# Kernel optimization log

Hardware: AMD Instinct MI355X
Metric: run time of the kernel (lower is better)

The kernel has to match this reference:

```python
import jax, jax.numpy as jnp
import numpy as np

B, S, D = 2, 2048, 1024
H, DQK, DV = 16, 64, 64
DECAY = 0.85


def _fractal_weights(seq_len: int, decay: float) -> np.ndarray:
    # Dragon-curve hierarchical weights: earlier (coarser) positions get higher
    # weight; weight decays by `decay` per hierarchy level. Normalized to sum 1,
    # matching DragonCurveGenerator.get_hierarchical_weights semantics.
    idx = np.arange(seq_len)
    level = np.floor(np.log2(idx + 1)).astype(np.int32)
    w = decay ** level.astype(np.float32)
    return (w / w.sum()).astype(np.float32)


def setup_inputs() -> dict:
    key = jax.random.key(0)
    kx, kq, kk, kv, ko = jax.random.split(key, 5)
    s = 1.0 / np.sqrt(D)
    return {
        "x": jax.random.normal(kx, (B, S, D), dtype=jnp.float32),
        "Wq": jax.random.normal(kq, (D, H * DQK), dtype=jnp.float32) * s,
        "Wk": jax.random.normal(kk, (D, H * DQK), dtype=jnp.float32) * s,
        "Wv": jax.random.normal(kv, (D, H * DV), dtype=jnp.float32) * s,
        "Wo": jax.random.normal(ko, (H * DV, D), dtype=jnp.float32) * s,
        "fractal_weights": jnp.asarray(_fractal_weights(S, DECAY)),
    }


def reference(x, Wq, Wk, Wv, Wo, fractal_weights):
    b, s, _ = x.shape
    # Projections (Linear with bias=False); weights stored as (in, out).
    Q = (x @ Wq).reshape(b, s, H, DQK).transpose(0, 2, 1, 3)  # [B,H,S,Dqk]
    K = (x @ Wk).reshape(b, s, H, DQK).transpose(0, 2, 1, 3)
    V = (x @ Wv).reshape(b, s, H, DV).transpose(0, 2, 1, 3)   # [B,H,S,Dv]
    scale = 1.0 / jnp.sqrt(jnp.asarray(DQK, dtype=x.dtype))
    scores = jnp.einsum("bhqd,bhkd->bhqk", Q, K) * scale      # [B,H,S,S]
    # Multiplicative per-key fractal bias applied BEFORE softmax.
    scores = scores * fractal_weights[None, None, None, :]
    attn = jax.nn.softmax(scores, axis=-1)
    out = jnp.einsum("bhqk,bhkd->bhqd", attn, V)               # [B,H,S,Dv]
    out = out.transpose(0, 2, 1, 3).reshape(b, s, H * DV)
    return out @ Wo                                            # [B,S,D]
```

## Files before the change

kernel.cpp:

```cpp
#include <hip/hip_runtime.h>
#include <hip/hip_bf16.h>
#include <stdint.h>

#define B_  2
#define S_  2048
#define D_  1024
#define H_  16
#define DH_ 64

typedef __attribute__((ext_vector_type(8))) __bf16    bf16x8;
typedef __attribute__((ext_vector_type(8))) _Float16  f16x8;
typedef __attribute__((ext_vector_type(2))) __fp16    fp16x2;
typedef __attribute__((ext_vector_type(4))) float     f32x4;

__device__ inline unsigned short f2bf(float f) {
    union { float f; uint32_t u; } v; v.f = f;
    uint32_t r = (v.u + 0x7fffu + ((v.u >> 16) & 1u)) >> 16;
    return (unsigned short)r;
}

__device__ __forceinline__ void g2l16(const unsigned short* g, unsigned short* l) {
    __builtin_amdgcn_global_load_lds(
        (const __attribute__((address_space(1))) unsigned int*)g,
        (__attribute__((address_space(3))) unsigned int*)l,
        16, 0, 0);
}


__global__ void convert_x(const float* __restrict__ x, unsigned short* __restrict__ xb, int n) {
    int i = (blockIdx.x * blockDim.x + threadIdx.x) * 4;
    if (i < n) {
        float4 v = *(const float4*)(x + i);
        ushort4 o;
        o.x = f2bf(v.x); o.y = f2bf(v.y); o.z = f2bf(v.z); o.w = f2bf(v.w);
        *(ushort4*)(xb + i) = o;
    }
}

__global__ void transpose_w(const float* __restrict__ s0, const float* __restrict__ s1,
                            const float* __restrict__ s2, const float* __restrict__ s3,
                            unsigned short* __restrict__ d0, unsigned short* __restrict__ d1,
                            unsigned short* __restrict__ d2, unsigned short* __restrict__ d3) {
    __shared__ float tile[32][33];
    const float* src; unsigned short* dst;
    switch (blockIdx.z) {
        case 0: src = s0; dst = d0; break;
        case 1: src = s1; dst = d1; break;
        case 2: src = s2; dst = d2; break;
        default: src = s3; dst = d3; break;
    }
    int n0 = blockIdx.x * 32, k0 = blockIdx.y * 32;
    int tx = threadIdx.x, ty = threadIdx.y;
    for (int j = 0; j < 32; j += 8)
        tile[ty + j][tx] = src[(long)(k0 + ty + j) * 1024 + n0 + tx];
    __syncthreads();
    for (int j = 0; j < 32; j += 8)
        dst[(long)(n0 + ty + j) * 1024 + k0 + tx] = f2bf(tile[tx][ty + j]);
}

template<int MODE>
__global__ __launch_bounds__(256, 2)
void gemm128(const unsigned short* __restrict__ A, const unsigned short* __restrict__ Bt,
             unsigned short* __restrict__ Qo, unsigned short* __restrict__ Ko,
             unsigned short* __restrict__ Vt, float* __restrict__ Cout)
{
    __shared__ __align__(16) unsigned short As[128 * 64];
    __shared__ __align__(16) unsigned short Bs[128 * 64];
    const int tid  = threadIdx.x;
    const int lane = tid & 63, wid = tid >> 6;
    const int quad = lane >> 4, l15 = lane & 15;
    const int wm = wid >> 1, wn = wid & 1;
    const int bm = blockIdx.y, bn = blockIdx.x;
    const int K = 1024;
    f32x4 acc[4][4] = {};
    const long Abase = (long)bm * 128 * K;
    const long Bbase = (long)bn * 128 * K;

    for (int k0 = 0; k0 < K; k0 += 64) {
        __syncthreads();
#pragma unroll
        for (int i = 0; i < 4; i++) {
            int slot = i * 256 + wid * 64 + lane;
            int row = slot >> 3, cp = slot & 7;
            int c = cp ^ (row & 7);
            g2l16(A + Abase + (long)row * K + k0 + c * 8, &As[(i * 256 + wid * 64) * 8]);
        }
#pragma unroll
        for (int i = 0; i < 4; i++) {
            int slot = i * 256 + wid * 64 + lane;
            int row = slot >> 3, cp = slot & 7;
            int c = cp ^ (row & 7);
            g2l16(Bt + Bbase + (long)row * K + k0 + c * 8, &Bs[(i * 256 + wid * 64) * 8]);
        }
        __syncthreads();
#pragma unroll
        for (int ks = 0; ks < 2; ks++) {
            bf16x8 af[4], bfr[4];
#pragma unroll
            for (int t = 0; t < 4; t++) {
                int ra = wm * 64 + t * 16 + l15;
                af[t]  = *(const bf16x8*)(As + ra * 64 + (((ks * 4 + quad) ^ (l15 & 7))) * 8);
                int rb = wn * 64 + t * 16 + l15;
                bfr[t] = *(const bf16x8*)(Bs + rb * 64 + (((ks * 4 + quad) ^ (l15 & 7))) * 8);
            }
#pragma unroll
            for (int tm = 0; tm < 4; tm++)
#pragma unroll
                for (int tn = 0; tn < 4; tn++)
                    acc[tm][tn] = __builtin_amdgcn_mfma_f32_16x16x32_bf16(af[tm], bfr[tn], acc[tm][tn], 0, 0, 0);
        }
    }

    const float Cq = 0.125f * 1.44269504f;
    for (int tm = 0; tm < 4; tm++)
        for (int tn = 0; tn < 4; tn++)
            for (int r = 0; r < 4; r++) {
                int gm = bm * 128 + wm * 64 + tm * 16 + quad * 4 + r;
                int gn = bn * 128 + wn * 64 + tn * 16 + l15;
                float v = acc[tm][tn][r];
                if (MODE == 0) {
                    int b = gm >> 11, s = gm & 2047;
                    if (gn < 1024) {
                        int h = gn >> 6, d = gn & 63;
                        Qo[(((long)(b * H_ + h) * S_ + s) << 6) + d] = f2bf(v * Cq);
                    } else if (gn < 2048) {
                        int g = gn - 1024; int h = g >> 6, d = g & 63;
                        Ko[(((long)(b * H_ + h) * S_ + s) << 6) + d] = f2bf(v);
                    } else {
                        int g = gn - 2048; int h = g >> 6, d = g & 63;
                        union { _Float16 h; unsigned short u; } cv;
                        cv.h = (_Float16)v;
                        Vt[((long)(b * H_ + h) * DH_ + d) * S_ + s] = cv.u;
                    }
                } else {
                    Cout[(long)gm * 1024 + gn] = v;
                }
            }
}

__global__ __launch_bounds__(256, 3)
void attn_kernel(const unsigned short* __restrict__ Q, const unsigned short* __restrict__ Kb,
                 const unsigned short* __restrict__ Vt, const float* __restrict__ fw,
                 unsigned short* __restrict__ O)
{
    __shared__ __align__(16) unsigned short Ks[2][64 * 64];
    __shared__ __align__(16) unsigned short Vs[2][64 * 64];
    __shared__ __align__(16) unsigned short P[4][32 * 72];

    const int tid  = threadIdx.x;
    const int lane = tid & 63, wid = tid >> 6;
    const int quad = lane >> 4, l15 = lane & 15;
    const int bh = blockIdx.y;
    const int qt = blockIdx.x;

    const unsigned short* Kg = Kb + (long)bh * S_ * DH_;
    const unsigned short* Vg = Vt + (long)bh * (long)DH_ * S_;

    bf16x8 qf[2][2];
#pragma unroll
    for (int s = 0; s < 2; s++) {
        const unsigned short* Qp = Q + ((long)bh * S_ + qt * 128 + wid * 32 + s * 16 + l15) * DH_ + quad * 8;
        qf[s][0] = *(const bf16x8*)(Qp);
        qf[s][1] = *(const bf16x8*)(Qp + 32);
    }

    auto issue = [&](int buf, int kt) {
#pragma unroll
        for (int i = 0; i < 2; i++) {
            int slot = wid * 128 + i * 64 + lane;
            int row = slot >> 3, cp = slot & 7;
            int c = cp ^ (row & 7);
            g2l16(Kg + ((long)(kt * 64 + row) * 64 + c * 8), &Ks[buf][(wid * 128 + i * 64) * 8]);
        }
#pragma unroll
        for (int i = 0; i < 2; i++) {
            int slot = wid * 128 + i * 64 + lane;
            int row = slot >> 3, cp = slot & 7;
            int c = cp ^ (row & 7);
            g2l16(Vg + ((long)row * S_ + kt * 64 + c * 8), &Vs[buf][(wid * 128 + i * 64) * 8]);
        }
    };

    f32x4 oacc[2][4] = {};
    float l_r[2] = {0.f, 0.f};

    issue(0, 0);
    __syncthreads();

    for (int kt = 0; kt < S_ / 64; kt++) {
        const int cur = kt & 1;
        if (kt + 1 < S_ / 64) issue(1 - cur, kt + 1);

        f32x4 wvc[4];
#pragma unroll
        for (int t = 0; t < 4; t++) {
            float4 w = *(const float4*)(fw + kt * 64 + t * 16 + quad * 4);
            wvc[t][0] = w.x; wvc[t][1] = w.y; wvc[t][2] = w.z; wvc[t][3] = w.w;
        }

        const unsigned short* Kc = &Ks[cur][0];
        const unsigned short* Vc = &Vs[cur][0];

        f32x4 sacc[2][4] = {};
#pragma unroll
        for (int t = 0; t < 4; t++) {
            int row = t * 16 + l15;
            bf16x8 k0 = *(const bf16x8*)(Kc + (row * 8 + (quad       ^ (l15 & 7))) * 8);
            bf16x8 k1 = *(const bf16x8*)(Kc + (row * 8 + ((4 + quad) ^ (l15 & 7))) * 8);
#pragma unroll
            for (int s = 0; s < 2; s++) {
                sacc[s][t] = __builtin_amdgcn_mfma_f32_16x16x32_bf16(k0, qf[s][0], sacc[s][t], 0, 0, 0);
                sacc[s][t] = __builtin_amdgcn_mfma_f32_16x16x32_bf16(k1, qf[s][1], sacc[s][t], 0, 0, 0);
            }
        }

        unsigned short* pb = &P[wid][0];
#pragma unroll
        for (int s = 0; s < 2; s++) {
#pragma unroll
            for (int t = 0; t < 4; t++) {
                float p0 = __builtin_amdgcn_exp2f(sacc[s][t][0] * wvc[t][0]);
                float p1 = __builtin_amdgcn_exp2f(sacc[s][t][1] * wvc[t][1]);
                float p2 = __builtin_amdgcn_exp2f(sacc[s][t][2] * wvc[t][2]);
                float p3 = __builtin_amdgcn_exp2f(sacc[s][t][3] * wvc[t][3]);
                l_r[s] += (p0 + p1) + (p2 + p3);
                union { fp16x2 h; unsigned int u; } a, b;
                a.h = __builtin_amdgcn_cvt_pkrtz(p0, p1);
                b.h = __builtin_amdgcn_cvt_pkrtz(p2, p3);
                *(uint2*)(pb + (s * 16 + l15) * 72 + t * 16 + quad * 4) = make_uint2(a.u, b.u);
            }
        }

#pragma unroll
        for (int ks = 0; ks < 2; ks++) {
            f16x8 pf0 = *(const f16x8*)(pb + l15 * 72 + ks * 32 + quad * 8);
            f16x8 pf1 = *(const f16x8*)(pb + (16 + l15) * 72 + ks * 32 + quad * 8);
#pragma unroll
            for (int t = 0; t < 4; t++) {
                int row = t * 16 + l15;
                f16x8 vf = *(const f16x8*)(Vc + (row * 8 + ((ks * 4 + quad) ^ (l15 & 7))) * 8);
                oacc[0][t] = __builtin_amdgcn_mfma_f32_16x16x32_f16(pf0, vf, oacc[0][t], 0, 0, 0);
                oacc[1][t] = __builtin_amdgcn_mfma_f32_16x16x32_f16(pf1, vf, oacc[1][t], 0, 0, 0);
            }
        }

        __syncthreads();
    }

#pragma unroll
    for (int s = 0; s < 2; s++) {
        l_r[s] += __shfl_xor(l_r[s], 16);
        l_r[s] += __shfl_xor(l_r[s], 32);
    }

    int b = bh >> 4, h = bh & 15;
#pragma unroll
    for (int s = 0; s < 2; s++)
#pragma unroll
        for (int r = 0; r < 4; r++) {
            float inv = 1.0f / __shfl(l_r[s], quad * 4 + r);
            int srow = qt * 128 + wid * 32 + s * 16 + quad * 4 + r;
#pragma unroll
            for (int t = 0; t < 4; t++)
                O[((long)(b * S_ + srow)) * 1024 + h * DH_ + t * 16 + l15] = f2bf(oacc[s][t][r] * inv);
        }
}


extern "C" void kernel_launch(void* const* d_in, const int* in_sizes, int n_in,
                              void* d_out, int out_size, void* d_ws, size_t ws_size,
                              hipStream_t stream)
{
    const float* x  = (const float*)d_in[0];
    const float* Wq = (const float*)d_in[1];
    const float* Wk = (const float*)d_in[2];
    const float* Wv = (const float*)d_in[3];
    const float* Wo = (const float*)d_in[4];
    const float* fw = (const float*)d_in[5];
    float* out = (float*)d_out;

    char* ws = (char*)d_ws;
    unsigned short* xb    = (unsigned short*)(ws);
    unsigned short* WqkvT = (unsigned short*)(ws + 8388608);
    unsigned short* WoT   = (unsigned short*)(ws + 14680064);
    unsigned short* Qb    = (unsigned short*)(ws + 16777216);
    unsigned short* Kb    = (unsigned short*)(ws + 25165824);
    unsigned short* Vt    = (unsigned short*)(ws + 33554432);
    unsigned short* Ob    = xb;

    convert_x<<<dim3((B_ * S_ * D_) / 4 / 256), dim3(256), 0, stream>>>(x, xb, B_ * S_ * D_);
    transpose_w<<<dim3(32, 32, 4), dim3(32, 8), 0, stream>>>(
        Wq, Wk, Wv, Wo,
        WqkvT, WqkvT + 1024 * 1024, WqkvT + 2 * 1024 * 1024, WoT);
    gemm128<0><<<dim3(24, 32), dim3(256), 0, stream>>>(xb, WqkvT, Qb, Kb, Vt, (float*)nullptr);
    attn_kernel<<<dim3(S_ / 128, B_ * H_), dim3(256), 0, stream>>>(Qb, Kb, Vt, fw, Ob);
    gemm128<1><<<dim3(8, 32), dim3(256), 0, stream>>>(Ob, WoT,
        (unsigned short*)nullptr, (unsigned short*)nullptr, (unsigned short*)nullptr, out);
}
```

Before: 208.2 us.

## Use two waves per attention block, each handling 64 query rows

The attention block drops from four waves to two, and each wave now processes 64 query rows instead of 32. K fragments are loaded from LDS once per tile and reused across four query subtiles, and each V fragment feeds four MFMAs, which cuts LDS reads per FLOP. The cost is fewer waves per block and more accumulator registers per thread (oacc 4x4), and the launch bounds change to (128,1). Occupancy and latency hiding may drop, and each wave now carries more of the global-to-LDS copy work.

```diff
diff --git a/kernel.cpp b/kernel.cpp
--- a/kernel.cpp
+++ b/kernel.cpp
@@ -138,14 +138,14 @@
             }
 }
 
-__global__ __launch_bounds__(256, 3)
+__global__ __launch_bounds__(128, 1)
 void attn_kernel(const unsigned short* __restrict__ Q, const unsigned short* __restrict__ Kb,
                  const unsigned short* __restrict__ Vt, const float* __restrict__ fw,
                  unsigned short* __restrict__ O)
 {
     __shared__ __align__(16) unsigned short Ks[2][64 * 64];
     __shared__ __align__(16) unsigned short Vs[2][64 * 64];
-    __shared__ __align__(16) unsigned short P[4][32 * 72];
+    __shared__ __align__(16) unsigned short P[2][64 * 72];
 
     const int tid  = threadIdx.x;
     const int lane = tid & 63, wid = tid >> 6;
@@ -156,33 +156,35 @@
     const unsigned short* Kg = Kb + (long)bh * S_ * DH_;
     const unsigned short* Vg = Vt + (long)bh * (long)DH_ * S_;
 
-    bf16x8 qf[2][2];
-#pragma unroll
-    for (int s = 0; s < 2; s++) {
-        const unsigned short* Qp = Q + ((long)bh * S_ + qt * 128 + wid * 32 + s * 16 + l15) * DH_ + quad * 8;
+    bf16x8 qf[4][2];
+#pragma unroll
+    for (int s = 0; s < 4; s++) {
+        const unsigned short* Qp = Q + ((long)bh * S_ + qt * 128 + wid * 64 + s * 16 + l15) * DH_ + quad * 8;
         qf[s][0] = *(const bf16x8*)(Qp);
         qf[s][1] = *(const bf16x8*)(Qp + 32);
     }
 
     auto issue = [&](int buf, int kt) {
 #pragma unroll
-        for (int i = 0; i < 2; i++) {
-            int slot = wid * 128 + i * 64 + lane;
+        for (int i = 0; i < 4; i++) {
+            int base = i * 128 + wid * 64;
+            int slot = base + lane;
             int row = slot >> 3, cp = slot & 7;
             int c = cp ^ (row & 7);
-            g2l16(Kg + ((long)(kt * 64 + row) * 64 + c * 8), &Ks[buf][(wid * 128 + i * 64) * 8]);
-        }
-#pragma unroll
-        for (int i = 0; i < 2; i++) {
-            int slot = wid * 128 + i * 64 + lane;
+            g2l16(Kg + ((long)(kt * 64 + row) * 64 + c * 8), &Ks[buf][base * 8]);
+        }
+#pragma unroll
+        for (int i = 0; i < 4; i++) {
+            int base = i * 128 + wid * 64;
+            int slot = base + lane;
             int row = slot >> 3, cp = slot & 7;
             int c = cp ^ (row & 7);
-            g2l16(Vg + ((long)row * S_ + kt * 64 + c * 8), &Vs[buf][(wid * 128 + i * 64) * 8]);
+            g2l16(Vg + ((long)row * S_ + kt * 64 + c * 8), &Vs[buf][base * 8]);
         }
     };
 
-    f32x4 oacc[2][4] = {};
-    float l_r[2] = {0.f, 0.f};
+    f32x4 oacc[4][4] = {};
+    float l_r[4] = {0.f, 0.f, 0.f, 0.f};
 
     issue(0, 0);
     __syncthreads();
@@ -201,28 +203,29 @@
         const unsigned short* Kc = &Ks[cur][0];
         const unsigned short* Vc = &Vs[cur][0];
 
-        f32x4 sacc[2][4] = {};
+        bf16x8 kf[4][2];
 #pragma unroll
         for (int t = 0; t < 4; t++) {
             int row = t * 16 + l15;
-            bf16x8 k0 = *(const bf16x8*)(Kc + (row * 8 + (quad       ^ (l15 & 7))) * 8);
-            bf16x8 k1 = *(const bf16x8*)(Kc + (row * 8 + ((4 + quad) ^ (l15 & 7))) * 8);
-#pragma unroll
-            for (int s = 0; s < 2; s++) {
-                sacc[s][t] = __builtin_amdgcn_mfma_f32_16x16x32_bf16(k0, qf[s][0], sacc[s][t], 0, 0, 0);
-                sacc[s][t] = __builtin_amdgcn_mfma_f32_16x16x32_bf16(k1, qf[s][1], sacc[s][t], 0, 0, 0);
-            }
+            kf[t][0] = *(const bf16x8*)(Kc + (row * 8 + (quad       ^ (l15 & 7))) * 8);
+            kf[t][1] = *(const bf16x8*)(Kc + (row * 8 + ((4 + quad) ^ (l15 & 7))) * 8);
         }
 
         unsigned short* pb = &P[wid][0];
 #pragma unroll
-        for (int s = 0; s < 2; s++) {
+        for (int s = 0; s < 4; s++) {
+            f32x4 sacc[4] = {};
 #pragma unroll
             for (int t = 0; t < 4; t++) {
-                float p0 = __builtin_amdgcn_exp2f(sacc[s][t][0] * wvc[t][0]);
-                float p1 = __builtin_amdgcn_exp2f(sacc[s][t][1] * wvc[t][1]);
-                float p2 = __builtin_amdgcn_exp2f(sacc[s][t][2] * wvc[t][2]);
-                float p3 = __builtin_amdgcn_exp2f(sacc[s][t][3] * wvc[t][3]);
+                sacc[t] = __builtin_amdgcn_mfma_f32_16x16x32_bf16(kf[t][0], qf[s][0], sacc[t], 0, 0, 0);
+                sacc[t] = __builtin_amdgcn_mfma_f32_16x16x32_bf16(kf[t][1], qf[s][1], sacc[t], 0, 0, 0);
+            }
+#pragma unroll
+            for (int t = 0; t < 4; t++) {
+                float p0 = __builtin_amdgcn_exp2f(sacc[t][0] * wvc[t][0]);
+                float p1 = __builtin_amdgcn_exp2f(sacc[t][1] * wvc[t][1]);
+                float p2 = __builtin_amdgcn_exp2f(sacc[t][2] * wvc[t][2]);
+                float p3 = __builtin_amdgcn_exp2f(sacc[t][3] * wvc[t][3]);
                 l_r[s] += (p0 + p1) + (p2 + p3);
                 union { fp16x2 h; unsigned int u; } a, b;
                 a.h = __builtin_amdgcn_cvt_pkrtz(p0, p1);
@@ -233,14 +236,17 @@
 
 #pragma unroll
         for (int ks = 0; ks < 2; ks++) {
-            f16x8 pf0 = *(const f16x8*)(pb + l15 * 72 + ks * 32 + quad * 8);
-            f16x8 pf1 = *(const f16x8*)(pb + (16 + l15) * 72 + ks * 32 + quad * 8);
+            f16x8 pf[4];
+#pragma unroll
+            for (int s = 0; s < 4; s++)
+                pf[s] = *(const f16x8*)(pb + (s * 16 + l15) * 72 + ks * 32 + quad * 8);
 #pragma unroll
             for (int t = 0; t < 4; t++) {
                 int row = t * 16 + l15;
                 f16x8 vf = *(const f16x8*)(Vc + (row * 8 + ((ks * 4 + quad) ^ (l15 & 7))) * 8);
-                oacc[0][t] = __builtin_amdgcn_mfma_f32_16x16x32_f16(pf0, vf, oacc[0][t], 0, 0, 0);
-                oacc[1][t] = __builtin_amdgcn_mfma_f32_16x16x32_f16(pf1, vf, oacc[1][t], 0, 0, 0);
+#pragma unroll
+                for (int s = 0; s < 4; s++)
+                    oacc[s][t] = __builtin_amdgcn_mfma_f32_16x16x32_f16(pf[s], vf, oacc[s][t], 0, 0, 0);
             }
         }
 
@@ -248,18 +254,18 @@
     }
 
 #pragma unroll
-    for (int s = 0; s < 2; s++) {
+    for (int s = 0; s < 4; s++) {
         l_r[s] += __shfl_xor(l_r[s], 16);
         l_r[s] += __shfl_xor(l_r[s], 32);
     }
 
     int b = bh >> 4, h = bh & 15;
 #pragma unroll
-    for (int s = 0; s < 2; s++)
+    for (int s = 0; s < 4; s++)
 #pragma unroll
         for (int r = 0; r < 4; r++) {
             float inv = 1.0f / __shfl(l_r[s], quad * 4 + r);
-            int srow = qt * 128 + wid * 32 + s * 16 + quad * 4 + r;
+            int srow = qt * 128 + wid * 64 + s * 16 + quad * 4 + r;
 #pragma unroll
             for (int t = 0; t < 4; t++)
                 O[((long)(b * S_ + srow)) * 1024 + h * DH_ + t * 16 + l15] = f2bf(oacc[s][t][r] * inv);
@@ -293,7 +299,7 @@
         Wq, Wk, Wv, Wo,
         WqkvT, WqkvT + 1024 * 1024, WqkvT + 2 * 1024 * 1024, WoT);
     gemm128<0><<<dim3(24, 32), dim3(256), 0, stream>>>(xb, WqkvT, Qb, Kb, Vt, (float*)nullptr);
-    attn_kernel<<<dim3(S_ / 128, B_ * H_), dim3(256), 0, stream>>>(Qb, Kb, Vt, fw, Ob);
+    attn_kernel<<<dim3(S_ / 128, B_ * H_), dim3(128), 0, stream>>>(Qb, Kb, Vt, fw, Ob);
     gemm128<1><<<dim3(8, 32), dim3(256), 0, stream>>>(Ob, WoT,
         (unsigned short*)nullptr, (unsigned short*)nullptr, (unsigned short*)nullptr, out);
 }
```

New measurement: 217.8 us. 4.6% more time.

## Feed softmax probabilities to PV MFMA directly from registers, skip LDS staging

Applied to the files above, without the earlier changes.

Drops the per-wave LDS buffer used to reshuffle the exponentiated scores. The S^T accumulator layout from the QK MFMA is reused directly as the A operand of 16x16x16 f16 MFMAs, with V fragments read at matching swizzled offsets. This removes LDS stores and loads plus their latency, at the cost of twice as many smaller-K MFMA issues. Occupancy hint drops from 3 to 2 blocks per SIMD-set, which gives more registers for the held probability fragments but may reduce latency hiding.

```diff
diff --git a/kernel.cpp b/kernel.cpp
--- a/kernel.cpp
+++ b/kernel.cpp
@@ -10,6 +10,7 @@
 
 typedef __attribute__((ext_vector_type(8))) __bf16    bf16x8;
 typedef __attribute__((ext_vector_type(8))) _Float16  f16x8;
+typedef __attribute__((ext_vector_type(4))) _Float16  f16x4;
 typedef __attribute__((ext_vector_type(2))) __fp16    fp16x2;
 typedef __attribute__((ext_vector_type(4))) float     f32x4;
 
@@ -138,14 +139,13 @@
             }
 }
 
-__global__ __launch_bounds__(256, 3)
+__global__ __launch_bounds__(256, 2)
 void attn_kernel(const unsigned short* __restrict__ Q, const unsigned short* __restrict__ Kb,
                  const unsigned short* __restrict__ Vt, const float* __restrict__ fw,
                  unsigned short* __restrict__ O)
 {
     __shared__ __align__(16) unsigned short Ks[2][64 * 64];
     __shared__ __align__(16) unsigned short Vs[2][64 * 64];
-    __shared__ __align__(16) unsigned short P[4][32 * 72];
 
     const int tid  = threadIdx.x;
     const int lane = tid & 63, wid = tid >> 6;
@@ -193,9 +193,9 @@
 
         f32x4 wvc[4];
 #pragma unroll
-        for (int t = 0; t < 4; t++) {
-            float4 w = *(const float4*)(fw + kt * 64 + t * 16 + quad * 4);
-            wvc[t][0] = w.x; wvc[t][1] = w.y; wvc[t][2] = w.z; wvc[t][3] = w.w;
+        for (int kc = 0; kc < 4; kc++) {
+            float4 w = *(const float4*)(fw + kt * 64 + kc * 16 + quad * 4);
+            wvc[kc][0] = w.x; wvc[kc][1] = w.y; wvc[kc][2] = w.z; wvc[kc][3] = w.w;
         }
 
         const unsigned short* Kc = &Ks[cur][0];
@@ -203,46 +203,45 @@
 
         f32x4 sacc[2][4] = {};
 #pragma unroll
-        for (int t = 0; t < 4; t++) {
-            int row = t * 16 + l15;
+        for (int kc = 0; kc < 4; kc++) {
+            int row = kc * 16 + l15;
             bf16x8 k0 = *(const bf16x8*)(Kc + (row * 8 + (quad       ^ (l15 & 7))) * 8);
             bf16x8 k1 = *(const bf16x8*)(Kc + (row * 8 + ((4 + quad) ^ (l15 & 7))) * 8);
 #pragma unroll
             for (int s = 0; s < 2; s++) {
-                sacc[s][t] = __builtin_amdgcn_mfma_f32_16x16x32_bf16(k0, qf[s][0], sacc[s][t], 0, 0, 0);
-                sacc[s][t] = __builtin_amdgcn_mfma_f32_16x16x32_bf16(k1, qf[s][1], sacc[s][t], 0, 0, 0);
-            }
-        }
-
-        unsigned short* pb = &P[wid][0];
-#pragma unroll
-        for (int s = 0; s < 2; s++) {
-#pragma unroll
-            for (int t = 0; t < 4; t++) {
-                float p0 = __builtin_amdgcn_exp2f(sacc[s][t][0] * wvc[t][0]);
-                float p1 = __builtin_amdgcn_exp2f(sacc[s][t][1] * wvc[t][1]);
-                float p2 = __builtin_amdgcn_exp2f(sacc[s][t][2] * wvc[t][2]);
-                float p3 = __builtin_amdgcn_exp2f(sacc[s][t][3] * wvc[t][3]);
+                sacc[s][kc] = __builtin_amdgcn_mfma_f32_16x16x32_bf16(k0, qf[s][0], sacc[s][kc], 0, 0, 0);
+                sacc[s][kc] = __builtin_amdgcn_mfma_f32_16x16x32_bf16(k1, qf[s][1], sacc[s][kc], 0, 0, 0);
+            }
+        }
+
+        f16x4 pk[2][4];
+#pragma unroll
+        for (int s = 0; s < 2; s++)
+#pragma unroll
+            for (int kc = 0; kc < 4; kc++) {
+                float p0 = __builtin_amdgcn_exp2f(sacc[s][kc][0] * wvc[kc][0]);
+                float p1 = __builtin_amdgcn_exp2f(sacc[s][kc][1] * wvc[kc][1]);
+                float p2 = __builtin_amdgcn_exp2f(sacc[s][kc][2] * wvc[kc][2]);
+                float p3 = __builtin_amdgcn_exp2f(sacc[s][kc][3] * wvc[kc][3]);
                 l_r[s] += (p0 + p1) + (p2 + p3);
                 union { fp16x2 h; unsigned int u; } a, b;
                 a.h = __builtin_amdgcn_cvt_pkrtz(p0, p1);
                 b.h = __builtin_amdgcn_cvt_pkrtz(p2, p3);
-                *(uint2*)(pb + (s * 16 + l15) * 72 + t * 16 + quad * 4) = make_uint2(a.u, b.u);
-            }
-        }
-
-#pragma unroll
-        for (int ks = 0; ks < 2; ks++) {
-            f16x8 pf0 = *(const f16x8*)(pb + l15 * 72 + ks * 32 + quad * 8);
-            f16x8 pf1 = *(const f16x8*)(pb + (16 + l15) * 72 + ks * 32 + quad * 8);
-#pragma unroll
-            for (int t = 0; t < 4; t++) {
-                int row = t * 16 + l15;
-                f16x8 vf = *(const f16x8*)(Vc + (row * 8 + ((ks * 4 + quad) ^ (l15 & 7))) * 8);
-                oacc[0][t] = __builtin_amdgcn_mfma_f32_16x16x32_f16(pf0, vf, oacc[0][t], 0, 0, 0);
-                oacc[1][t] = __builtin_amdgcn_mfma_f32_16x16x32_f16(pf1, vf, oacc[1][t], 0, 0, 0);
-            }
-        }
+                union { uint2 u; f16x4 v; } pku;
+                pku.u = make_uint2(a.u, b.u);
+                pk[s][kc] = pku.v;
+            }
+
+#pragma unroll
+        for (int kc = 0; kc < 4; kc++)
+#pragma unroll
+            for (int dt = 0; dt < 4; dt++) {
+                int row = dt * 16 + l15;
+                int pos = (kc * 2 + (quad >> 1)) ^ (l15 & 7);
+                f16x4 vf = *(const f16x4*)(Vc + row * 64 + pos * 8 + (quad & 1) * 4);
+                oacc[0][dt] = __builtin_amdgcn_mfma_f32_16x16x16f16(pk[0][kc], vf, oacc[0][dt], 0, 0, 0);
+                oacc[1][dt] = __builtin_amdgcn_mfma_f32_16x16x16f16(pk[1][kc], vf, oacc[1][dt], 0, 0, 0);
+            }
 
         __syncthreads();
     }
@@ -261,8 +260,8 @@
             float inv = 1.0f / __shfl(l_r[s], quad * 4 + r);
             int srow = qt * 128 + wid * 32 + s * 16 + quad * 4 + r;
 #pragma unroll
-            for (int t = 0; t < 4; t++)
-                O[((long)(b * S_ + srow)) * 1024 + h * DH_ + t * 16 + l15] = f2bf(oacc[s][t][r] * inv);
+            for (int dt = 0; dt < 4; dt++)
+                O[((long)(b * S_ + srow)) * 1024 + h * DH_ + dt * 16 + l15] = f2bf(oacc[s][dt][r] * inv);
         }
 }
 
```

New measurement: 212.5 us. 1.02x slower.
